# Optimization experiments

Hardware: AMD Instinct MI355X
Metric: run time of the kernel (lower is better)

## Reference

```python
import jax, jax.numpy as jnp
import numpy as np

NUM_HEADS = 8
EPS = 1e-9


def setup_inputs() -> dict:
    key = jax.random.key(0)
    ks = jax.random.split(key, 5)
    B, S, D = 2, 2048, 512
    x = jax.random.normal(ks[0], (B, S, D), dtype=jnp.float32)
    Wq = jax.random.normal(ks[1], (D, D), dtype=jnp.float32) * (1.0 / np.sqrt(D))
    Wk = jax.random.normal(ks[2], (D, D), dtype=jnp.float32) * (1.0 / np.sqrt(D))
    Wv = jax.random.normal(ks[3], (D, D), dtype=jnp.float32) * (1.0 / np.sqrt(D))
    Wo = jax.random.normal(ks[4], (D, D), dtype=jnp.float32) * (1.0 / np.sqrt(D))
    gamma = jnp.ones((D,), dtype=jnp.float32)
    beta = jnp.zeros((D,), dtype=jnp.float32)
    return {"x": x, "Wq": Wq, "Wk": Wk, "Wv": Wv, "Wo": Wo, "gamma": gamma, "beta": beta}


def _layernorm(x, gamma, beta):
    mean = jnp.mean(x, axis=-1, keepdims=True)
    var = jnp.mean(jnp.square(x - mean), axis=-1, keepdims=True)
    return gamma * ((x - mean) * jax.lax.rsqrt(var + EPS)) + beta


def reference(x, Wq, Wk, Wv, Wo, gamma, beta):
    B, S, D = x.shape
    H = NUM_HEADS
    dh = D // H
    # Note: in the original, K_V=(inputs, inputs) is captured BEFORE LayerNorm,
    # so only Q is layer-normalized; K and V use the raw inputs.
    q_in = _layernorm(x, gamma, beta)
    Q = jnp.einsum('bsd,de->bse', q_in, Wq).reshape(B, S, H, dh)
    K = jnp.einsum('bsd,de->bse', x, Wk).reshape(B, S, H, dh)
    V = jnp.einsum('bsd,de->bse', x, Wv).reshape(B, S, H, dh)
    # scaled dot-product attention (bias = 0, dropout disabled since dropout=1)
    scores = jnp.einsum('bqhd,bkhd->bhqk', Q, K) / jnp.sqrt(jnp.float32(dh))
    attn = jax.nn.softmax(scores, axis=-1)
    ctx = jnp.einsum('bhqk,bkhd->bqhd', attn, V).reshape(B, S, D)
    out = jnp.einsum('bsd,de->bse', ctx, Wo) + x  # output proj + residual
    return out
```

## Files before the change

### kernel.cpp

```cpp
#include <hip/hip_runtime.h>

typedef __bf16 bf16x8 __attribute__((ext_vector_type(8)));
typedef float f32x4 __attribute__((ext_vector_type(4)));

#define SCALE_LOG2E 0.18033688011112042f

__device__ __forceinline__ float bf2f(unsigned int u) { return __uint_as_float(u << 16); }
__device__ __forceinline__ unsigned short f2bfu(float f) {
    union { __bf16 h; unsigned short u; } v;
    v.h = (__bf16)f;
    return v.u;
}
__device__ __forceinline__ unsigned int pk2bf(float a, float b) {
    union { __bf16 h[2]; unsigned int u; } v;
    v.h[0] = (__bf16)a; v.h[1] = (__bf16)b;
    return v.u;
}

__device__ int probe_bf16(const void* xp) {
    const unsigned short* u = (const unsigned short*)xp;
    int cnt = 0;
    for (int i = 0; i < 128; i++) {
        unsigned e = (u[i] >> 7) & 0xFFu;
        cnt += (e == 0u || (e >= 0x6Cu && e <= 0x8Au)) ? 1 : 0;
    }
    return cnt >= 120;
}

__global__ __launch_bounds__(64)
void probe_k(const void* __restrict__ x, const void* __restrict__ Wq, int* __restrict__ flags) {
    if (threadIdx.x == 0) {
        flags[0] = probe_bf16(x);
        flags[1] = probe_bf16(Wq);
    }
}

__device__ __forceinline__ void load8f(const void* p, int isb, size_t idx, float* o) {
    if (isb) {
        uint4 v = *(const uint4*)((const unsigned short*)p + idx);
        o[0] = bf2f(v.x & 0xffffu); o[1] = bf2f(v.x >> 16);
        o[2] = bf2f(v.y & 0xffffu); o[3] = bf2f(v.y >> 16);
        o[4] = bf2f(v.z & 0xffffu); o[5] = bf2f(v.z >> 16);
        o[6] = bf2f(v.w & 0xffffu); o[7] = bf2f(v.w >> 16);
    } else {
        const float* f = (const float*)p + idx;
        float4 a = *(const float4*)f;
        float4 b = *(const float4*)(f + 4);
        o[0] = a.x; o[1] = a.y; o[2] = a.z; o[3] = a.w;
        o[4] = b.x; o[5] = b.y; o[6] = b.z; o[7] = b.w;
    }
}
__device__ __forceinline__ void load2f(const void* p, int isb, size_t idx, float& a, float& b) {
    if (isb) {
        unsigned int v = *(const unsigned int*)((const unsigned short*)p + idx);
        a = bf2f(v & 0xffffu); b = bf2f(v >> 16);
    } else {
        float2 f = *(const float2*)((const float*)p + idx);
        a = f.x; b = f.y;
    }
}
__device__ __forceinline__ float load1f(const void* p, int isb, size_t idx) {
    return isb ? bf2f((unsigned int)((const unsigned short*)p)[idx]) : ((const float*)p)[idx];
}

__global__ __launch_bounds__(256)
void setup_k(const void* __restrict__ x, const void* __restrict__ Wq, const void* __restrict__ Wk,
             const void* __restrict__ Wv, const void* __restrict__ Wo,
             const void* __restrict__ gamma, const void* __restrict__ beta,
             float* __restrict__ rowstats, float* __restrict__ gf, float* __restrict__ bfv,
             unsigned short* __restrict__ WT, const int* __restrict__ flags) {
    const int t = threadIdx.x;
    const int bid = blockIdx.x;
    if (bid < 1024) {
        const int isb = flags[1];
        __shared__ float tile[32][33];
        const int which = bid >> 8, tl = bid & 255;
        const int bx = (tl & 15) * 32, by = (tl >> 4) * 32;
        const void* W = (which == 0) ? Wq : (which == 1) ? Wk : (which == 2) ? Wv : Wo;
        unsigned short* dst = WT + (size_t)which * 512 * 512;
        const int xx = t & 31, y0 = t >> 5;
#pragma unroll
        for (int i = 0; i < 4; i++) {
            int y = y0 + i * 8;
            tile[y][xx] = load1f(W, isb, (size_t)(by + y) * 512 + bx + xx);
        }
        __syncthreads();
#pragma unroll
        for (int i = 0; i < 4; i++) {
            int y = y0 + i * 8;
            dst[(size_t)(bx + y) * 512 + by + xx] = f2bfu(tile[xx][y]);
        }
        return;
    }
    const int isb = flags[0];
    if (bid >= 5120) {
        const void* src = (bid == 5120) ? gamma : beta;
        float* dst = (bid == 5120) ? gf : bfv;
        float a, b;
        load2f(src, isb, (size_t)t * 2, a, b);
        dst[t * 2] = a; dst[t * 2 + 1] = b;
        return;
    }
    const int row = bid - 1024;
    float a, b;
    load2f(x, isb, (size_t)row * 512 + t * 2, a, b);
    float s = a + b, sq = a * a + b * b;
#pragma unroll
    for (int msk = 1; msk < 64; msk <<= 1) {
        s += __shfl_xor(s, msk);
        sq += __shfl_xor(sq, msk);
    }
    __shared__ float red[8];
    if ((t & 63) == 0) { red[t >> 6] = s; red[4 + (t >> 6)] = sq; }
    __syncthreads();
    if (t == 0) {
        float S = red[0] + red[1] + red[2] + red[3];
        float SQ = red[4] + red[5] + red[6] + red[7];
        float mean = S * (1.0f / 512.0f);
        float var = SQ * (1.0f / 512.0f) - mean * mean;
        rowstats[2 * row] = mean;
        rowstats[2 * row + 1] = rsqrtf(fmaxf(var, 0.0f) + 1e-9f);
    }
}

__global__ __launch_bounds__(256)
void proj_all_k(const void* __restrict__ x, const unsigned short* __restrict__ WT,
                const float* __restrict__ rowstats, const float* __restrict__ gf,
                const float* __restrict__ bfv, unsigned short* __restrict__ Qb,
                unsigned short* __restrict__ Kb, unsigned short* __restrict__ VtF,
                const int* __restrict__ flags) {
    __shared__ unsigned short As[128 * 40];
    __shared__ unsigned short Bs[128 * 40];
    __shared__ float Gs[512], Bts[512];
    const int t = threadIdx.x;
    const int isb = flags[0];
    const int w = t >> 6, lane = t & 63;
    const int quad = lane >> 4, ln = lane & 15;

    if (blockIdx.z == 0) {
        const int role = blockIdx.x & 1;
        const int n0 = (blockIdx.x >> 1) * 128;
        const int m0 = blockIdx.y * 128;
        const unsigned short* BT = WT + (size_t)role * 512 * 512;
        unsigned short* out = role ? Kb : Qb;
        const int wm = w & 1, wn = w >> 1;
        Gs[t] = gf[t]; Gs[t + 256] = gf[t + 256];
        Bts[t] = bfv[t]; Bts[t + 256] = bfv[t + 256];

        f32x4 acc[4][4];
        const f32x4 zero = {0.f, 0.f, 0.f, 0.f};
#pragma unroll
        for (int i = 0; i < 4; i++)
#pragma unroll
            for (int j = 0; j < 4; j++) acc[i][j] = zero;

        for (int kt = 0; kt < 512; kt += 32) {
            __syncthreads();
#pragma unroll
            for (int i = 0; i < 2; i++) {
                int o = t + i * 256;
                int r = o >> 2, c8 = o & 3;
                size_t gidx = (size_t)(m0 + r) * 512 + kt + c8 * 8;
                if (isb && role == 1) {
                    *(uint4*)(&As[r * 40 + c8 * 8]) = *(const uint4*)((const unsigned short*)x + gidx);
                } else {
                    float f[8];
                    load8f(x, isb, gidx, f);
                    if (role == 0) {
                        float mean = rowstats[2 * (m0 + r)];
                        float inv = rowstats[2 * (m0 + r) + 1];
#pragma unroll
                        for (int j = 0; j < 8; j++) {
                            int k = kt + c8 * 8 + j;
                            f[j] = (f[j] - mean) * inv * Gs[k] + Bts[k];
                        }
                    }
                    unsigned int pk[4];
#pragma unroll
                    for (int j = 0; j < 4; j++) pk[j] = pk2bf(f[2 * j], f[2 * j + 1]);
                    *(uint4*)(&As[r * 40 + c8 * 8]) = make_uint4(pk[0], pk[1], pk[2], pk[3]);
                }
                *(uint4*)(&Bs[r * 40 + c8 * 8]) = *(const uint4*)(BT + (size_t)(n0 + r) * 512 + kt + c8 * 8);
            }
            __syncthreads();
            bf16x8 af[4], bfr[4];
#pragma unroll
            for (int i = 0; i < 4; i++) {
                af[i] = *(const bf16x8*)(&As[(wm * 64 + i * 16 + ln) * 40 + quad * 8]);
                bfr[i] = *(const bf16x8*)(&Bs[(wn * 64 + i * 16 + ln) * 40 + quad * 8]);
            }
#pragma unroll
            for (int i = 0; i < 4; i++)
#pragma unroll
                for (int j = 0; j < 4; j++)
                    acc[i][j] = __builtin_amdgcn_mfma_f32_16x16x32_bf16(af[i], bfr[j], acc[i][j], 0, 0, 0);
        }
#pragma unroll
        for (int i = 0; i < 4; i++)
#pragma unroll
            for (int j = 0; j < 4; j++)
#pragma unroll
                for (int r = 0; r < 4; r++) {
                    int grow = m0 + wm * 64 + i * 16 + quad * 4 + r;
                    int gcol = n0 + wn * 64 + j * 16 + ln;
                    float v = acc[i][j][r];
                    if (role == 0) v *= SCALE_LOG2E;
                    out[(size_t)grow * 512 + gcol] = f2bfu(v);
                }
    } else {
        const int m0 = blockIdx.x * 64;
        const int n0 = blockIdx.y * 128;
        const unsigned short* AW = WT + (size_t)2 * 512 * 512;

        f32x4 acc[8];
        const f32x4 zero = {0.f, 0.f, 0.f, 0.f};
#pragma unroll
        for (int j = 0; j < 8; j++) acc[j] = zero;

        for (int kt = 0; kt < 512; kt += 32) {
            __syncthreads();
            {
                int r = t >> 2, c8 = t & 3;
                *(uint4*)(&As[r * 40 + c8 * 8]) = *(const uint4*)(AW + (size_t)(m0 + r) * 512 + kt + c8 * 8);
            }
#pragma unroll
            for (int i = 0; i < 2; i++) {
                int o = t + i * 256;
                int r = o >> 2, c8 = o & 3;
                size_t gidx = (size_t)(n0 + r) * 512 + kt + c8 * 8;
                if (isb) {
                    *(uint4*)(&Bs[r * 40 + c8 * 8]) = *(const uint4*)((const unsigned short*)x + gidx);
                } else {
                    float f[8];
                    load8f(x, isb, gidx, f);
                    unsigned int pk[4];
#pragma unroll
                    for (int j = 0; j < 4; j++) pk[j] = pk2bf(f[2 * j], f[2 * j + 1]);
                    *(uint4*)(&Bs[r * 40 + c8 * 8]) = make_uint4(pk[0], pk[1], pk[2], pk[3]);
                }
            }
            __syncthreads();
            bf16x8 af = *(const bf16x8*)(&As[(w * 16 + ln) * 40 + quad * 8]);
#pragma unroll
            for (int j = 0; j < 8; j++) {
                bf16x8 bfr = *(const bf16x8*)(&Bs[(j * 16 + ln) * 40 + quad * 8]);
                acc[j] = __builtin_amdgcn_mfma_f32_16x16x32_bf16(af, bfr, acc[j], 0, 0, 0);
            }
        }
#pragma unroll
        for (int j = 0; j < 8; j++)
#pragma unroll
            for (int r = 0; r < 4; r++) {
                int grow = m0 + w * 16 + quad * 4 + r;
                int gcol = n0 + j * 16 + ln;
                VtF[(size_t)grow * 4096 + gcol] = f2bfu(acc[j][r]);
            }
    }
}

__global__ __launch_bounds__(512, 4)
void attn_m_k(const unsigned short* __restrict__ Qb, const unsigned short* __restrict__ Kb,
              const unsigned short* __restrict__ VtF, unsigned short* __restrict__ ctx) {
    const int S = 2048, PT = 72, NT = 32;
    const int t = threadIdx.x;
    const int qb = blockIdx.x, h = blockIdx.y, b = blockIdx.z;
    const int w = t >> 6, lane = t & 63;
    const int quad = lane >> 4, ln = lane & 15;
    const int kq = w & 3, qh = w >> 2;

    __shared__ unsigned short sh[32256];
    unsigned short* const Qs  = sh;
    unsigned short* const KsA = sh + 4608;
    unsigned short* const KsB = sh + 9216;
    unsigned short* const Vt0 = sh + 13824;
    unsigned short* const Vt1 = sh + 18432;
    unsigned short* const Vt2 = sh + 23040;
    unsigned short* const Vt3 = sh + 27648;

    const size_t baseQ  = (size_t)(b * S + qb * 64) * 512 + h * 64;
    const size_t baseK  = (size_t)(b * S) * 512 + h * 64;
    const size_t baseVt = (size_t)(h * 64) * 4096 + (size_t)b * S;

    const int c8 = t & 7;
    const int isK = t < 256;
    const int rS = (t & 255) >> 3;
    const int stoff0 = rS * PT + c8 * 8;
    const int stoff1 = (rS + 32) * PT + c8 * 8;

    const int kfo0 = (kq * 16 + ln) * PT + quad * 8;
    const int vto  = ln * PT + kq * 16 + quad * 4;

    const unsigned short* const gK = Kb + baseK + (size_t)rS * 512 + c8 * 8;
    const unsigned short* const gV = VtF + baseVt + (size_t)rS * 4096 + c8 * 8;

    uint4 sa0, sa1, sb0, sb1;
    if (isK) {
        sa0 = *(const uint4*)(gK);          sa1 = *(const uint4*)(gK + 16384);
        sb0 = *(const uint4*)(gK + 32768);  sb1 = *(const uint4*)(gK + 49152);
    } else {
        sa0 = *(const uint4*)(gV);          sa1 = *(const uint4*)(gV + 131072);
        sb0 = *(const uint4*)(gV + 64);     sb1 = *(const uint4*)(gV + 64 + 131072);
    }

    {
        const int rQ = t >> 3;
        *(uint4*)(&Qs[rQ * PT + c8 * 8]) = *(const uint4*)(Qb + baseQ + (size_t)rQ * 512 + c8 * 8);
    }
    __syncthreads();
    bf16x8 qf[2][2];
#pragma unroll
    for (int s2 = 0; s2 < 2; s2++)
#pragma unroll
        for (int i = 0; i < 2; i++)
            qf[s2][i] = *(const bf16x8*)(&Qs[(qh * 32 + s2 * 16 + ln) * PT + quad * 8 + 32 * i]);

    f32x4 acc[2][4];
    const f32x4 zero = {0.f, 0.f, 0.f, 0.f};
#pragma unroll
    for (int s2 = 0; s2 < 2; s2++)
#pragma unroll
        for (int j = 0; j < 4; j++) acc[s2][j] = zero;
    float lsum0 = 0.f, lsum1 = 0.f;

#define STAGE(KS, VT, R0, R1)                                               \
    {                                                                       \
        if (isK) { *(uint4*)(&KS[stoff0]) = R0; *(uint4*)(&KS[stoff1]) = R1; } \
        else     { *(uint4*)(&VT[stoff0]) = R0; *(uint4*)(&VT[stoff1]) = R1; } \
    }
#define PRELOAD(R0, R1, kt)                                                 \
    if ((kt) < NT) {                                                        \
        if (isK) {                                                          \
            R0 = *(const uint4*)(gK + (size_t)(kt) * 32768);                \
            R1 = *(const uint4*)(gK + (size_t)(kt) * 32768 + 16384);        \
        } else {                                                            \
            R0 = *(const uint4*)(gV + (size_t)(kt) * 64);                   \
            R1 = *(const uint4*)(gV + (size_t)(kt) * 64 + 131072);          \
        }                                                                   \
    }
#define QK_EXP(KS, U00, U01, U10, U11)                                      \
    {                                                                       \
        bf16x8 kf0 = *(const bf16x8*)(&KS[kfo0]);                           \
        bf16x8 kf1 = *(const bf16x8*)(&KS[kfo0 + 32]);                      \
        f32x4 sc0 = zero, sc1 = zero;                                       \
        sc0 = __builtin_amdgcn_mfma_f32_16x16x32_bf16(kf0, qf[0][0], sc0, 0, 0, 0); \
        sc0 = __builtin_amdgcn_mfma_f32_16x16x32_bf16(kf1, qf[0][1], sc0, 0, 0, 0); \
        sc1 = __builtin_amdgcn_mfma_f32_16x16x32_bf16(kf0, qf[1][0], sc1, 0, 0, 0); \
        sc1 = __builtin_amdgcn_mfma_f32_16x16x32_bf16(kf1, qf[1][1], sc1, 0, 0, 0); \
        float a0 = __builtin_amdgcn_exp2f(fminf(sc0[0], 30.f));             \
        float a1 = __builtin_amdgcn_exp2f(fminf(sc0[1], 30.f));             \
        float a2 = __builtin_amdgcn_exp2f(fminf(sc0[2], 30.f));             \
        float a3 = __builtin_amdgcn_exp2f(fminf(sc0[3], 30.f));             \
        lsum0 += (a0 + a1) + (a2 + a3);                                     \
        U00 = pk2bf(a0, a1); U01 = pk2bf(a2, a3);                           \
        float b0 = __builtin_amdgcn_exp2f(fminf(sc1[0], 30.f));             \
        float b1 = __builtin_amdgcn_exp2f(fminf(sc1[1], 30.f));             \
        float b2 = __builtin_amdgcn_exp2f(fminf(sc1[2], 30.f));             \
        float b3 = __builtin_amdgcn_exp2f(fminf(sc1[3], 30.f));             \
        lsum1 += (b0 + b1) + (b2 + b3);                                     \
        U10 = pk2bf(b0, b1); U11 = pk2bf(b2, b3);                           \
    }
#define PV4(VTE, VTO)                                                       \
    {                                                                       \
        bf16x8 ap0 = __builtin_bit_cast(bf16x8, make_uint4(uA00, uA01, uB00, uB01)); \
        bf16x8 ap1 = __builtin_bit_cast(bf16x8, make_uint4(uA10, uA11, uB10, uB11)); \
        _Pragma("unroll")                                                   \
        for (int nt = 0; nt < 4; nt++) {                                    \
            uint2 ve = *(const uint2*)(&VTE[vto + nt * 16 * PT]);           \
            uint2 vo = *(const uint2*)(&VTO[vto + nt * 16 * PT]);           \
            bf16x8 vb = __builtin_bit_cast(bf16x8, make_uint4(ve.x, ve.y, vo.x, vo.y)); \
            acc[0][nt] = __builtin_amdgcn_mfma_f32_16x16x32_bf16(ap0, vb, acc[0][nt], 0, 0, 0); \
            acc[1][nt] = __builtin_amdgcn_mfma_f32_16x16x32_bf16(ap1, vb, acc[1][nt], 0, 0, 0); \
        }                                                                   \
    }

    for (int m = 0; m < 8; m++) {
        const int T = m * 4;
        unsigned int uA00, uA01, uA10, uA11, uB00, uB01, uB10, uB11;
        STAGE(KsA, Vt0, sa0, sa1);
        __syncthreads();
        PRELOAD(sa0, sa1, T + 2);
        QK_EXP(KsA, uA00, uA01, uA10, uA11);
        STAGE(KsB, Vt1, sb0, sb1);
        __syncthreads();
        PRELOAD(sb0, sb1, T + 3);
        QK_EXP(KsB, uB00, uB01, uB10, uB11);
        PV4(Vt0, Vt1);
        __syncthreads();
        STAGE(KsA, Vt2, sa0, sa1);
        __syncthreads();
        PRELOAD(sa0, sa1, T + 4);
        QK_EXP(KsA, uA00, uA01, uA10, uA11);
        STAGE(KsB, Vt3, sb0, sb1);
        __syncthreads();
        PRELOAD(sb0, sb1, T + 5);
        QK_EXP(KsB, uB00, uB01, uB10, uB11);
        PV4(Vt2, Vt3);
        __syncthreads();
    }
#undef STAGE
#undef PRELOAD
#undef QK_EXP
#undef PV4

    lsum0 += __shfl_xor(lsum0, 16);
    lsum0 += __shfl_xor(lsum0, 32);
    lsum1 += __shfl_xor(lsum1, 16);
    lsum1 += __shfl_xor(lsum1, 32);

    __syncthreads();
    float* scr  = (float*)sh;
    float* lred = scr + 13056;
    if (quad == 0) {
        lred[kq * 64 + qh * 32 + ln] = lsum0;
        lred[kq * 64 + qh * 32 + 16 + ln] = lsum1;
    }
    if (kq != 0) {
        const int pb = (kq - 1) * 4352 + (qh * 32 + quad * 4) * 68 + ln;
#pragma unroll
        for (int s2 = 0; s2 < 2; s2++)
#pragma unroll
            for (int nt = 0; nt < 4; nt++)
#pragma unroll
                for (int r = 0; r < 4; r++)
                    scr[pb + (s2 * 16 + r) * 68 + nt * 16] = acc[s2][nt][r];
    }
    __syncthreads();
    if (kq == 0) {
#pragma unroll
        for (int s2 = 0; s2 < 2; s2++) {
            const size_t baseO = (size_t)(b * S + qb * 64 + qh * 32 + s2 * 16 + quad * 4) * 512 + h * 64 + ln;
#pragma unroll
            for (int r = 0; r < 4; r++) {
                int qrow = qh * 32 + s2 * 16 + quad * 4 + r;
                float lt = lred[qrow] + lred[64 + qrow] + lred[128 + qrow] + lred[192 + qrow];
                float inv = 1.0f / lt;
                int rb = qrow * 68 + ln;
#pragma unroll
                for (int nt = 0; nt < 4; nt++) {
                    float v = acc[s2][nt][r] + scr[rb + nt * 16] + scr[4352 + rb + nt * 16] + scr[8704 + rb + nt * 16];
                    ctx[baseO + (size_t)r * 512 + nt * 16] = f2bfu(v * inv);
                }
            }
        }
    }
}

__global__ __launch_bounds__(256)
void outproj_k(const unsigned short* __restrict__ ctx, const unsigned short* __restrict__ BT,
               const void* __restrict__ x, void* __restrict__ outp, const int* __restrict__ flags) {
    __shared__ unsigned short As[128 * 40];
    __shared__ unsigned short Bs[64 * 40];
    const int t = threadIdx.x;
    const int isb = flags[0];
    const int m0 = blockIdx.y * 128, n0 = blockIdx.x * 64;
    const int w = t >> 6, lane = t & 63;
    const int wm = w & 1, wn = w >> 1;
    const int quad = lane >> 4, ln = lane & 15;

    f32x4 acc[4][2];
    const f32x4 zero = {0.f, 0.f, 0.f, 0.f};
#pragma unroll
    for (int i = 0; i < 4; i++)
#pragma unroll
        for (int j = 0; j < 2; j++) acc[i][j] = zero;

    for (int kt = 0; kt < 512; kt += 32) {
        __syncthreads();
#pragma unroll
        for (int i = 0; i < 2; i++) {
            int o = t + i * 256;
            int r = o >> 2, c8 = o & 3;
            *(uint4*)(&As[r * 40 + c8 * 8]) = *(const uint4*)(ctx + (size_t)(m0 + r) * 512 + kt + c8 * 8);
        }
        {
            int r = t >> 2, c8 = t & 3;
            *(uint4*)(&Bs[r * 40 + c8 * 8]) = *(const uint4*)(BT + (size_t)(n0 + r) * 512 + kt + c8 * 8);
        }
        __syncthreads();
        bf16x8 af[4], bfr[2];
#pragma unroll
        for (int i = 0; i < 4; i++)
            af[i] = *(const bf16x8*)(&As[(wm * 64 + i * 16 + ln) * 40 + quad * 8]);
#pragma unroll
        for (int j = 0; j < 2; j++)
            bfr[j] = *(const bf16x8*)(&Bs[(wn * 32 + j * 16 + ln) * 40 + quad * 8]);
#pragma unroll
        for (int i = 0; i < 4; i++)
#pragma unroll
            for (int j = 0; j < 2; j++)
                acc[i][j] = __builtin_amdgcn_mfma_f32_16x16x32_bf16(af[i], bfr[j], acc[i][j], 0, 0, 0);
    }
#pragma unroll
    for (int i = 0; i < 4; i++)
#pragma unroll
        for (int j = 0; j < 2; j++)
#pragma unroll
            for (int r = 0; r < 4; r++) {
                int grow = m0 + wm * 64 + i * 16 + quad * 4 + r;
                int gcol = n0 + wn * 32 + j * 16 + ln;
                size_t idx = (size_t)grow * 512 + gcol;
                float v = acc[i][j][r] + load1f(x, isb, idx);
                if (isb) ((unsigned short*)outp)[idx] = f2bfu(v);
                else     ((float*)outp)[idx] = v;
            }
}

__global__ __launch_bounds__(256)
void fill_k(unsigned short* out, int n) {
    int i = blockIdx.x * 256 + threadIdx.x;
    if (i < n) out[i] = 0x4442;
}

extern "C" void kernel_launch(void* const* d_in, const int* in_sizes, int n_in,
                              void* d_out, int out_size, void* d_ws, size_t ws_size,
                              hipStream_t stream) {
    const void* x     = d_in[0];
    const void* Wq    = d_in[1];
    const void* Wk    = d_in[2];
    const void* Wv    = d_in[3];
    const void* Wo    = d_in[4];
    const void* gamma = d_in[5];
    const void* beta  = d_in[6];

    const size_t NW = 512 * 512;
    const size_t NX = 4096 * 512;
    char* w = (char*)d_ws;

    const size_t FULL_STATS_OFF = 2097152 + 3 * NX * 2;
    const size_t NEED_FULL = FULL_STATS_OFF + 32768 + 4096 + 16;

    if (ws_size < NEED_FULL) {
        fill_k<<<(out_size + 255) / 256, 256, 0, stream>>>((unsigned short*)d_out, out_size);
        return;
    }

    unsigned short* WT  = (unsigned short*)w;
    unsigned short* Qb  = (unsigned short*)(w + 2097152);
    unsigned short* Kb  = Qb + NX;
    unsigned short* VtF = Kb + NX;
    unsigned short* ctx = Qb;
    float* rowstats = (float*)(w + FULL_STATS_OFF);
    float* gf = rowstats + 8192;
    float* bfv = gf + 512;
    int* flags = (int*)(bfv + 512);

    probe_k<<<1, 64, 0, stream>>>(x, Wq, flags);
    setup_k<<<5122, 256, 0, stream>>>(x, Wq, Wk, Wv, Wo, gamma, beta, rowstats, gf, bfv, WT, flags);
    proj_all_k<<<dim3(8, 32, 2), 256, 0, stream>>>(x, WT, rowstats, gf, bfv, Qb, Kb, VtF, flags);
    attn_m_k<<<dim3(32, 8, 2), 512, 0, stream>>>(Qb, Kb, VtF, ctx);
    outproj_k<<<dim3(8, 32), 256, 0, stream>>>(ctx, WT + 3 * NW, x, d_out, flags);
}
```

Before: 162.8 us.

## Double attention query tile to 128 rows with 1024-thread blocks, drop syncs

The attention kernel now processes 128 query rows per block using 1024 threads (16 waves), so each staged K/V tile is reused by twice as many queries and global K/V traffic per query is halved. Each thread now stages one 16-byte chunk per tile instead of two. The Q staging buffer overlaps a V buffer, which cuts LDS use, and two barriers per loop iteration are removed by relying on the buffer rotation order. The partial-sum reduction runs in two rounds so the shared scratch stays small. The grid halves to 256 blocks, which cuts parallelism and latency hiding, and makes every barrier cover 16 waves.

```diff
diff --git a/kernel.cpp b/kernel.cpp
--- a/kernel.cpp
+++ b/kernel.cpp
@@ -258,7 +258,7 @@
     }
 }
 
-__global__ __launch_bounds__(512, 4)
+__global__ __launch_bounds__(1024, 1)
 void attn_m_k(const unsigned short* __restrict__ Qb, const unsigned short* __restrict__ Kb,
               const unsigned short* __restrict__ VtF, unsigned short* __restrict__ ctx) {
     const int S = 2048, PT = 72, NT = 32;
@@ -268,39 +268,32 @@
     const int quad = lane >> 4, ln = lane & 15;
     const int kq = w & 3, qh = w >> 2;
 
-    __shared__ unsigned short sh[32256];
-    unsigned short* const Qs  = sh;
-    unsigned short* const KsA = sh + 4608;
-    unsigned short* const KsB = sh + 9216;
-    unsigned short* const Vt0 = sh + 13824;
-    unsigned short* const Vt1 = sh + 18432;
-    unsigned short* const Vt2 = sh + 23040;
-    unsigned short* const Vt3 = sh + 27648;
-
-    const size_t baseQ  = (size_t)(b * S + qb * 64) * 512 + h * 64;
+    __shared__ unsigned short sh[27648];
+    unsigned short* const KsA = sh;
+    unsigned short* const KsB = sh + 4608;
+    unsigned short* const Vt0 = sh + 9216;
+    unsigned short* const Vt1 = sh + 13824;
+    unsigned short* const Vt2 = sh + 18432;
+    unsigned short* const Vt3 = sh + 23040;
+    unsigned short* const Qs  = sh + 18432;
+
+    const size_t baseQ  = (size_t)(b * S + qb * 128) * 512 + h * 64;
     const size_t baseK  = (size_t)(b * S) * 512 + h * 64;
     const size_t baseVt = (size_t)(h * 64) * 4096 + (size_t)b * S;
 
     const int c8 = t & 7;
-    const int isK = t < 256;
-    const int rS = (t & 255) >> 3;
-    const int stoff0 = rS * PT + c8 * 8;
-    const int stoff1 = (rS + 32) * PT + c8 * 8;
+    const int r64 = (t & 511) >> 3;
+    const int stoff = r64 * PT + c8 * 8;
 
     const int kfo0 = (kq * 16 + ln) * PT + quad * 8;
     const int vto  = ln * PT + kq * 16 + quad * 4;
 
-    const unsigned short* const gK = Kb + baseK + (size_t)rS * 512 + c8 * 8;
-    const unsigned short* const gV = VtF + baseVt + (size_t)rS * 4096 + c8 * 8;
-
-    uint4 sa0, sa1, sb0, sb1;
-    if (isK) {
-        sa0 = *(const uint4*)(gK);          sa1 = *(const uint4*)(gK + 16384);
-        sb0 = *(const uint4*)(gK + 32768);  sb1 = *(const uint4*)(gK + 49152);
-    } else {
-        sa0 = *(const uint4*)(gV);          sa1 = *(const uint4*)(gV + 131072);
-        sb0 = *(const uint4*)(gV + 64);     sb1 = *(const uint4*)(gV + 64 + 131072);
-    }
+    const unsigned short* const gK = Kb + baseK + (size_t)r64 * 512 + c8 * 8;
+    const unsigned short* const gV = VtF + baseVt + (size_t)r64 * 4096 + c8 * 8;
+
+    uint4 sa, sb;
+    if (t < 512) { sa = *(const uint4*)(gK); sb = *(const uint4*)(gK + 32768); }
+    else         { sa = *(const uint4*)(gV); sb = *(const uint4*)(gV + 64); }
 
     {
         const int rQ = t >> 3;
@@ -322,20 +315,15 @@
         for (int j = 0; j < 4; j++) acc[s2][j] = zero;
     float lsum0 = 0.f, lsum1 = 0.f;
 
-#define STAGE(KS, VT, R0, R1)                                               \
+#define STAGE(KS, VT, R)                                                    \
     {                                                                       \
-        if (isK) { *(uint4*)(&KS[stoff0]) = R0; *(uint4*)(&KS[stoff1]) = R1; } \
-        else     { *(uint4*)(&VT[stoff0]) = R0; *(uint4*)(&VT[stoff1]) = R1; } \
-    }
-#define PRELOAD(R0, R1, kt)                                                 \
+        if (t < 512) *(uint4*)(&KS[stoff]) = R;                             \
+        else         *(uint4*)(&VT[stoff]) = R;                             \
+    }
+#define PRELOAD(R, kt)                                                      \
     if ((kt) < NT) {                                                        \
-        if (isK) {                                                          \
-            R0 = *(const uint4*)(gK + (size_t)(kt) * 32768);                \
-            R1 = *(const uint4*)(gK + (size_t)(kt) * 32768 + 16384);        \
-        } else {                                                            \
-            R0 = *(const uint4*)(gV + (size_t)(kt) * 64);                   \
-            R1 = *(const uint4*)(gV + (size_t)(kt) * 64 + 131072);          \
-        }                                                                   \
+        if (t < 512) R = *(const uint4*)(gK + (size_t)(kt) * 32768);        \
+        else         R = *(const uint4*)(gV + (size_t)(kt) * 64);           \
     }
 #define QK_EXP(KS, U00, U01, U10, U11)                                      \
     {                                                                       \
@@ -376,26 +364,24 @@
     for (int m = 0; m < 8; m++) {
         const int T = m * 4;
         unsigned int uA00, uA01, uA10, uA11, uB00, uB01, uB10, uB11;
-        STAGE(KsA, Vt0, sa0, sa1);
-        __syncthreads();
-        PRELOAD(sa0, sa1, T + 2);
+        STAGE(KsA, Vt0, sa);
+        __syncthreads();
+        PRELOAD(sa, T + 2);
         QK_EXP(KsA, uA00, uA01, uA10, uA11);
-        STAGE(KsB, Vt1, sb0, sb1);
-        __syncthreads();
-        PRELOAD(sb0, sb1, T + 3);
+        STAGE(KsB, Vt1, sb);
+        __syncthreads();
+        PRELOAD(sb, T + 3);
         QK_EXP(KsB, uB00, uB01, uB10, uB11);
         PV4(Vt0, Vt1);
-        __syncthreads();
-        STAGE(KsA, Vt2, sa0, sa1);
-        __syncthreads();
-        PRELOAD(sa0, sa1, T + 4);
+        STAGE(KsA, Vt2, sa);
+        __syncthreads();
+        PRELOAD(sa, T + 4);
         QK_EXP(KsA, uA00, uA01, uA10, uA11);
-        STAGE(KsB, Vt3, sb0, sb1);
-        __syncthreads();
-        PRELOAD(sb0, sb1, T + 5);
+        STAGE(KsB, Vt3, sb);
+        __syncthreads();
+        PRELOAD(sb, T + 5);
         QK_EXP(KsB, uB00, uB01, uB10, uB11);
         PV4(Vt2, Vt3);
-        __syncthreads();
     }
 #undef STAGE
 #undef PRELOAD
@@ -411,34 +397,38 @@
     float* scr  = (float*)sh;
     float* lred = scr + 13056;
     if (quad == 0) {
-        lred[kq * 64 + qh * 32 + ln] = lsum0;
-        lred[kq * 64 + qh * 32 + 16 + ln] = lsum1;
-    }
-    if (kq != 0) {
-        const int pb = (kq - 1) * 4352 + (qh * 32 + quad * 4) * 68 + ln;
-#pragma unroll
-        for (int s2 = 0; s2 < 2; s2++)
-#pragma unroll
-            for (int nt = 0; nt < 4; nt++)
-#pragma unroll
-                for (int r = 0; r < 4; r++)
-                    scr[pb + (s2 * 16 + r) * 68 + nt * 16] = acc[s2][nt][r];
-    }
-    __syncthreads();
-    if (kq == 0) {
-#pragma unroll
-        for (int s2 = 0; s2 < 2; s2++) {
-            const size_t baseO = (size_t)(b * S + qb * 64 + qh * 32 + s2 * 16 + quad * 4) * 512 + h * 64 + ln;
-#pragma unroll
-            for (int r = 0; r < 4; r++) {
-                int qrow = qh * 32 + s2 * 16 + quad * 4 + r;
-                float lt = lred[qrow] + lred[64 + qrow] + lred[128 + qrow] + lred[192 + qrow];
-                float inv = 1.0f / lt;
-                int rb = qrow * 68 + ln;
-#pragma unroll
-                for (int nt = 0; nt < 4; nt++) {
-                    float v = acc[s2][nt][r] + scr[rb + nt * 16] + scr[4352 + rb + nt * 16] + scr[8704 + rb + nt * 16];
-                    ctx[baseO + (size_t)r * 512 + nt * 16] = f2bfu(v * inv);
+        lred[kq * 128 + qh * 32 + ln] = lsum0;
+        lred[kq * 128 + qh * 32 + 16 + ln] = lsum1;
+    }
+#pragma unroll
+    for (int rr = 0; rr < 2; rr++) {
+        __syncthreads();
+        if ((qh >> 1) == rr && kq != 0) {
+            const int pb = (kq - 1) * 4352 + ((qh & 1) * 32 + quad * 4) * 68 + ln;
+#pragma unroll
+            for (int s2 = 0; s2 < 2; s2++)
+#pragma unroll
+                for (int nt = 0; nt < 4; nt++)
+#pragma unroll
+                    for (int r = 0; r < 4; r++)
+                        scr[pb + (s2 * 16 + r) * 68 + nt * 16] = acc[s2][nt][r];
+        }
+        __syncthreads();
+        if ((qh >> 1) == rr && kq == 0) {
+#pragma unroll
+            for (int s2 = 0; s2 < 2; s2++) {
+                const size_t baseO = (size_t)(b * S + qb * 128 + qh * 32 + s2 * 16 + quad * 4) * 512 + h * 64 + ln;
+#pragma unroll
+                for (int r = 0; r < 4; r++) {
+                    int qrow = qh * 32 + s2 * 16 + quad * 4 + r;
+                    float lt = lred[qrow] + lred[128 + qrow] + lred[256 + qrow] + lred[384 + qrow];
+                    float inv = 1.0f / lt;
+                    int rb = ((qh & 1) * 32 + s2 * 16 + quad * 4 + r) * 68 + ln;
+#pragma unroll
+                    for (int nt = 0; nt < 4; nt++) {
+                        float v = acc[s2][nt][r] + scr[rb + nt * 16] + scr[4352 + rb + nt * 16] + scr[8704 + rb + nt * 16];
+                        ctx[baseO + (size_t)r * 512 + nt * 16] = f2bfu(v * inv);
+                    }
                 }
             }
         }
@@ -547,6 +537,6 @@
     probe_k<<<1, 64, 0, stream>>>(x, Wq, flags);
     setup_k<<<5122, 256, 0, stream>>>(x, Wq, Wk, Wv, Wo, gamma, beta, rowstats, gf, bfv, WT, flags);
     proj_all_k<<<dim3(8, 32, 2), 256, 0, stream>>>(x, WT, rowstats, gf, bfv, Qb, Kb, VtF, flags);
-    attn_m_k<<<dim3(32, 8, 2), 512, 0, stream>>>(Qb, Kb, VtF, ctx);
+    attn_m_k<<<dim3(16, 8, 2), 1024, 0, stream>>>(Qb, Kb, VtF, ctx);
     outproj_k<<<dim3(8, 32), 256, 0, stream>>>(ctx, WT + 3 * NW, x, d_out, flags);
 }
```

Result: no change. 161.0 us (-1.1%).
